# Kernel optimization log

Hardware: AMD Instinct MI355X
Metric: run time of the kernel (lower is better)

Reference implementation:

```python
import jax, jax.numpy as jnp
import numpy as np
import math

PHI = (1.0 + math.sqrt(5.0)) / 2.0
LUT_SIZE = 4096
TWO_PI = 2.0 * math.pi


def _lut_tables():
    # 4096-entry sin/cos lookup tables over [0, 2*pi)
    grid = jnp.arange(LUT_SIZE, dtype=jnp.float32) * (TWO_PI / LUT_SIZE)
    return jnp.sin(grid), jnp.cos(grid)


def _lookup_sin_cos(theta, sin_t, cos_t):
    # nearest-entry LUT lookup: index = round(theta / (2*pi) * N) mod N
    idx = jnp.mod(jnp.round(theta * (LUT_SIZE / TWO_PI)), LUT_SIZE).astype(jnp.int32)
    return sin_t[idx], cos_t[idx]


def setup_inputs() -> dict:
    key = jax.random.key(0)
    ks = jax.random.split(key, 6)
    B, D, H = 16, 2048, 2048
    return {
        "current_state_real": jax.random.normal(ks[0], (B, D), jnp.float32),
        "current_state_imag": jax.random.normal(ks[1], (B, D), jnp.float32),
        "history_real": jax.random.normal(ks[2], (B, H, D), jnp.float32),
        "history_imag": jax.random.normal(ks[3], (B, H, D), jnp.float32),
        "ema_state": jax.random.normal(ks[4], (B, 2 * D), jnp.float32),
        "w_q": jax.random.normal(ks[5], (D,), jnp.float32) * 0.02,
        "b_q": jnp.zeros((D,), jnp.float32),
        "alpha": jnp.asarray(0.1, jnp.float32),
        "t": jnp.asarray(3.0, jnp.float32),
    }


def reference(current_state_real, current_state_imag, history_real, history_imag,
              ema_state, w_q, b_q, alpha, t):
    D = current_state_real.shape[-1]
    scale = math.sqrt(2.0 * D)
    sin_t, cos_t = _lut_tables()

    wl_q = 1.0 + jnp.abs(w_q)                      # (D,)
    t_phi = t * PHI
    theta_real = current_state_real / wl_q + b_q + t_phi   # (B, D)
    theta_imag = current_state_imag / wl_q + b_q + t_phi   # (B, D)
    _, cos_q_real = _lookup_sin_cos(theta_real, sin_t, cos_t)
    _, cos_q_imag = _lookup_sin_cos(theta_imag, sin_t, cos_t)

    # keys == values == stacked history (no projection): (B, H, 2D)
    keys = jnp.concatenate([history_real, history_imag], axis=-1)
    query_for_match = jnp.concatenate([cos_q_real, cos_q_imag], axis=-1)  # (B, 2D)

    scores = jnp.einsum('bd,bhd->bh', query_for_match, keys) / scale      # (B, H)
    weights = jax.nn.softmax(scores, axis=-1)
    retrieved = jnp.einsum('bh,bhd->bd', weights, keys)                   # (B, 2D)

    a = jax.nn.sigmoid(alpha)
    new_ema = a * retrieved + (1.0 - a) * ema_state
    return new_ema
```

## Files before the change

kernel.cpp:

```cpp
#include <hip/hip_runtime.h>
#include <math.h>

#ifndef M_PI
#define M_PI 3.14159265358979323846
#endif

#define LUT_N 4096

__device__ __forceinline__ float lut_cos(float theta) {
    const float IDX_SCALE = (float)((double)LUT_N / (2.0 * M_PI));
    const float STEP = (float)((2.0 * M_PI) / (double)LUT_N);
    float x = theta * IDX_SCALE;
    int i = (int)rintf(x);
    i &= (LUT_N - 1);
    return cosf((float)i * STEP);
}

__global__ void qgen_kernel(const float* __restrict__ cur_r,
                            const float* __restrict__ cur_i,
                            const float* __restrict__ w_q,
                            const float* __restrict__ b_q,
                            const float* __restrict__ t_ptr,
                            float* __restrict__ q_out,
                            int B, int D) {
    int idx = blockIdx.x * blockDim.x + threadIdx.x;
    int twoD = 2 * D;
    if (idx >= B * twoD) return;
    int b = idx / twoD;
    int c = idx - b * twoD;
    int col = (c < D) ? c : c - D;
    const float* src = (c < D) ? cur_r : cur_i;
    float v = src[(size_t)b * D + col];
    float t_phi = t_ptr[0] * 1.61803398874989484820f;
    float wl = 1.0f + fabsf(w_q[col]);
    float theta = v / wl + b_q[col] + t_phi;
    q_out[idx] = lut_cos(theta);
}

__global__ __launch_bounds__(256) void flash_kernel(
    const float* __restrict__ hist_r,
    const float* __restrict__ hist_i,
    const float* __restrict__ q_ws,
    float* __restrict__ r_ws,
    float* __restrict__ ml_ws,
    int H, int D, int S) {
    const int t = threadIdx.x;
    const int b = blockIdx.x / S;
    const int s = blockIdx.x - b * S;
    const int rows = H / S;
    const int h0 = s * rows;
    const int Dv = D >> 2;

    const float4* qv4 = (const float4*)q_ws + (size_t)b * (D >> 1);
    float4 qv[4], rv[4];
#pragma unroll
    for (int j = 0; j < 4; ++j) {
        qv[j] = qv4[t + 256 * j];
        rv[j] = make_float4(0.f, 0.f, 0.f, 0.f);
    }
    const float4* hr4 = (const float4*)hist_r + (size_t)b * H * Dv;
    const float4* hi4 = (const float4*)hist_i + (size_t)b * H * Dv;

    float m = -INFINITY, l = 0.0f;
    const float inv_scale = 1.0f / sqrtf(2.0f * (float)D);
    __shared__ float red[4];

    for (int hh = 0; hh < rows; ++hh) {
        const size_t ro = (size_t)(h0 + hh) * Dv;
        float4 kv[4];
        kv[0] = hr4[ro + t];
        kv[1] = hr4[ro + t + 256];
        kv[2] = hi4[ro + t];
        kv[3] = hi4[ro + t + 256];
        float p = 0.f;
#pragma unroll
        for (int j = 0; j < 4; ++j)
            p += qv[j].x * kv[j].x + qv[j].y * kv[j].y +
                 qv[j].z * kv[j].z + qv[j].w * kv[j].w;
#pragma unroll
        for (int off = 32; off > 0; off >>= 1) p += __shfl_down(p, off);
        if ((t & 63) == 0) red[t >> 6] = p;
        __syncthreads();
        float sc = (red[0] + red[1] + red[2] + red[3]) * inv_scale;
        __syncthreads();
        float m_new = fmaxf(m, sc);
        float corr = expf(m - m_new);
        float w = expf(sc - m_new);
        l = fmaf(l, corr, w);
#pragma unroll
        for (int j = 0; j < 4; ++j) {
            rv[j].x = fmaf(rv[j].x, corr, w * kv[j].x);
            rv[j].y = fmaf(rv[j].y, corr, w * kv[j].y);
            rv[j].z = fmaf(rv[j].z, corr, w * kv[j].z);
            rv[j].w = fmaf(rv[j].w, corr, w * kv[j].w);
        }
        m = m_new;
    }
    float4* rout = (float4*)r_ws + (size_t)(b * S + s) * (D >> 1);
#pragma unroll
    for (int j = 0; j < 4; ++j) rout[t + 256 * j] = rv[j];
    if (t == 0) {
        ml_ws[(size_t)(b * S + s) * 2] = m;
        ml_ws[(size_t)(b * S + s) * 2 + 1] = l;
    }
}

__global__ void combine_kernel(const float* __restrict__ r_ws,
                               const float* __restrict__ ml_ws,
                               const float* __restrict__ ema,
                               const float* __restrict__ alpha_ptr,
                               float* __restrict__ out,
                               int D, int S) {
    const int twoD = 2 * D;
    const int nc = twoD / 256;
    const int b = blockIdx.x / nc;
    const int cb = blockIdx.x - b * nc;
    const int c = cb * 256 + threadIdx.x;

    const float* ml = ml_ws + (size_t)b * S * 2;
    float M = -INFINITY;
    for (int s = 0; s < S; ++s) M = fmaxf(M, ml[2 * s]);
    float L = 0.f;
    for (int s = 0; s < S; ++s) L += ml[2 * s + 1] * expf(ml[2 * s] - M);

    float acc = 0.f;
    const float* rb = r_ws + (size_t)b * S * twoD + c;
    for (int s = 0; s < S; ++s)
        acc = fmaf(expf(ml[2 * s] - M), rb[(size_t)s * twoD], acc);

    float a = 1.0f / (1.0f + expf(-alpha_ptr[0]));
    float retrieved = acc / L;
    size_t o = (size_t)b * twoD + c;
    out[o] = a * retrieved + (1.0f - a) * ema[o];
}

extern "C" void kernel_launch(void* const* d_in, const int* in_sizes, int n_in,
                              void* d_out, int out_size, void* d_ws, size_t ws_size,
                              hipStream_t stream) {
    const float* cur_r  = (const float*)d_in[0];
    const float* cur_i  = (const float*)d_in[1];
    const float* hist_r = (const float*)d_in[2];
    const float* hist_i = (const float*)d_in[3];
    const float* ema    = (const float*)d_in[4];
    const float* w_q    = (const float*)d_in[5];
    const float* b_q    = (const float*)d_in[6];
    const float* alpha  = (const float*)d_in[7];
    const float* t      = (const float*)d_in[8];

    const int D = in_sizes[5];
    const int B = in_sizes[0] / D;
    const int H = in_sizes[2] / (B * D);
    const int twoD = 2 * D;

    float* q_ws = (float*)d_ws;
    size_t q_elems = (size_t)B * twoD;

    int S = 64;
    while (S > 1) {
        size_t need = (q_elems + (size_t)B * S * twoD + (size_t)B * S * 2) * sizeof(float);
        if (need <= ws_size) break;
        S >>= 1;
    }
    float* r_ws = q_ws + q_elems;
    float* ml_ws = r_ws + (size_t)B * S * twoD;

    int qblocks = (B * twoD + 255) / 256;
    qgen_kernel<<<qblocks, 256, 0, stream>>>(cur_r, cur_i, w_q, b_q, t, q_ws, B, D);
    flash_kernel<<<B * S, 256, 0, stream>>>(hist_r, hist_i, q_ws, r_ws, ml_ws, H, D, S);
    combine_kernel<<<B * (twoD / 256), 256, 0, stream>>>(r_ws, ml_ws, ema, alpha,
                                                         (float*)d_out, D, S);
}
```

Before: 139.2 us.

## Widen flash kernel to 1024 threads and batch rows per barrier

The split-softmax attention kernel now uses 1024-thread blocks, each thread owning one float4 of the 2D row, and processes four history rows per barrier using double-buffered shared partial sums. The aim is to cut the per-row __syncthreads cost and to keep more independent loads in flight. The split count drops from 64 to 32 to keep the block count reasonable. D is now hardcoded to 2048 (the scale is fixed at 1/64 and the row stride at 512 float4s), and the loop assumes rows divisible by 4, so other shapes would break.

```diff
diff --git a/kernel.cpp b/kernel.cpp
--- a/kernel.cpp
+++ b/kernel.cpp
@@ -6,6 +6,7 @@
 #endif
 
 #define LUT_N 4096
+#define RBATCH 4
 
 __device__ __forceinline__ float lut_cos(float theta) {
     const float IDX_SCALE = (float)((double)LUT_N / (2.0 * M_PI));
@@ -37,68 +38,72 @@
     q_out[idx] = lut_cos(theta);
 }
 
-__global__ __launch_bounds__(256) void flash_kernel(
+__global__ __launch_bounds__(1024, 8) void flash_kernel(
     const float* __restrict__ hist_r,
     const float* __restrict__ hist_i,
     const float* __restrict__ q_ws,
     float* __restrict__ r_ws,
     float* __restrict__ ml_ws,
-    int H, int D, int S) {
+    int H, int S) {
     const int t = threadIdx.x;
     const int b = blockIdx.x / S;
     const int s = blockIdx.x - b * S;
     const int rows = H / S;
     const int h0 = s * rows;
-    const int Dv = D >> 2;
 
-    const float4* qv4 = (const float4*)q_ws + (size_t)b * (D >> 1);
-    float4 qv[4], rv[4];
+    const int half = t >> 9;
+    const int cc = t & 511;
+    const int wave = t >> 6, lane = t & 63;
+
+    const float4* base = (const float4*)(half ? hist_i : hist_r)
+                         + ((size_t)b * H + h0) * 512 + cc;
+    float4 qv = ((const float4*)q_ws)[(size_t)b * 1024 + t];
+    float4 rv = make_float4(0.f, 0.f, 0.f, 0.f);
+    float m = -INFINITY, l = 0.0f;
+    const float inv_scale = 1.0f / 64.0f;
+
+    __shared__ float part[2][RBATCH][16];
+
+    const int nb = rows / RBATCH;
+    for (int kb = 0; kb < nb; ++kb) {
+        const float4* rp = base + (size_t)(kb * RBATCH) * 512;
+        float4 kv[RBATCH];
 #pragma unroll
-    for (int j = 0; j < 4; ++j) {
-        qv[j] = qv4[t + 256 * j];
-        rv[j] = make_float4(0.f, 0.f, 0.f, 0.f);
+        for (int i = 0; i < RBATCH; ++i) kv[i] = rp[(size_t)i * 512];
+
+#pragma unroll
+        for (int i = 0; i < RBATCH; ++i) {
+            float p = qv.x * kv[i].x + qv.y * kv[i].y +
+                      qv.z * kv[i].z + qv.w * kv[i].w;
+#pragma unroll
+            for (int off = 32; off > 0; off >>= 1) p += __shfl_down(p, off);
+            if (lane == 0) part[kb & 1][i][wave] = p;
+        }
+        __syncthreads();
+
+        const float4* pp = (const float4*)part[kb & 1];
+#pragma unroll
+        for (int i = 0; i < RBATCH; ++i) {
+            float4 a0 = pp[4 * i + 0], a1 = pp[4 * i + 1];
+            float4 a2 = pp[4 * i + 2], a3 = pp[4 * i + 3];
+            float sc = ((a0.x + a0.y) + (a0.z + a0.w)) +
+                       ((a1.x + a1.y) + (a1.z + a1.w)) +
+                       ((a2.x + a2.y) + (a2.z + a2.w)) +
+                       ((a3.x + a3.y) + (a3.z + a3.w));
+            sc *= inv_scale;
+            float m_new = fmaxf(m, sc);
+            float corr = expf(m - m_new);
+            float w = expf(sc - m_new);
+            l = fmaf(l, corr, w);
+            rv.x = fmaf(rv.x, corr, w * kv[i].x);
+            rv.y = fmaf(rv.y, corr, w * kv[i].y);
+            rv.z = fmaf(rv.z, corr, w * kv[i].z);
+            rv.w = fmaf(rv.w, corr, w * kv[i].w);
+            m = m_new;
+        }
     }
-    const float4* hr4 = (const float4*)hist_r + (size_t)b * H * Dv;
-    const float4* hi4 = (const float4*)hist_i + (size_t)b * H * Dv;
 
-    float m = -INFINITY, l = 0.0f;
-    const float inv_scale = 1.0f / sqrtf(2.0f * (float)D);
-    __shared__ float red[4];
-
-    for (int hh = 0; hh < rows; ++hh) {
-        const size_t ro = (size_t)(h0 + hh) * Dv;
-        float4 kv[4];
-        kv[0] = hr4[ro + t];
-        kv[1] = hr4[ro + t + 256];
-        kv[2] = hi4[ro + t];
-        kv[3] = hi4[ro + t + 256];
-        float p = 0.f;
-#pragma unroll
-        for (int j = 0; j < 4; ++j)
-            p += qv[j].x * kv[j].x + qv[j].y * kv[j].y +
-                 qv[j].z * kv[j].z + qv[j].w * kv[j].w;
-#pragma unroll
-        for (int off = 32; off > 0; off >>= 1) p += __shfl_down(p, off);
-        if ((t & 63) == 0) red[t >> 6] = p;
-        __syncthreads();
-        float sc = (red[0] + red[1] + red[2] + red[3]) * inv_scale;
-        __syncthreads();
-        float m_new = fmaxf(m, sc);
-        float corr = expf(m - m_new);
-        float w = expf(sc - m_new);
-        l = fmaf(l, corr, w);
-#pragma unroll
-        for (int j = 0; j < 4; ++j) {
-            rv[j].x = fmaf(rv[j].x, corr, w * kv[j].x);
-            rv[j].y = fmaf(rv[j].y, corr, w * kv[j].y);
-            rv[j].z = fmaf(rv[j].z, corr, w * kv[j].z);
-            rv[j].w = fmaf(rv[j].w, corr, w * kv[j].w);
-        }
-        m = m_new;
-    }
-    float4* rout = (float4*)r_ws + (size_t)(b * S + s) * (D >> 1);
-#pragma unroll
-    for (int j = 0; j < 4; ++j) rout[t + 256 * j] = rv[j];
+    ((float4*)r_ws)[(size_t)(b * S + s) * 1024 + t] = rv;
     if (t == 0) {
         ml_ws[(size_t)(b * S + s) * 2] = m;
         ml_ws[(size_t)(b * S + s) * 2 + 1] = l;
@@ -155,7 +160,7 @@
     float* q_ws = (float*)d_ws;
     size_t q_elems = (size_t)B * twoD;
 
-    int S = 64;
+    int S = 32;
     while (S > 1) {
         size_t need = (q_elems + (size_t)B * S * twoD + (size_t)B * S * 2) * sizeof(float);
         if (need <= ws_size) break;
@@ -166,7 +171,7 @@
 
     int qblocks = (B * twoD + 255) / 256;
     qgen_kernel<<<qblocks, 256, 0, stream>>>(cur_r, cur_i, w_q, b_q, t, q_ws, B, D);
-    flash_kernel<<<B * S, 256, 0, stream>>>(hist_r, hist_i, q_ws, r_ws, ml_ws, H, D, S);
+    flash_kernel<<<B * S, 1024, 0, stream>>>(hist_r, hist_i, q_ws, r_ws, ml_ws, H, S);
     combine_kernel<<<B * (twoD / 256), 256, 0, stream>>>(r_ws, ml_ws, ema, alpha,
                                                          (float*)d_out, D, S);
 }
```

New measurement: 124.1 us. 1.12x faster.

## Give each wavefront its own history rows in flash attention, removing per-row block syncs

Applied to the files above, without the earlier changes.

The flash kernel now assigns disjoint row ranges to each of four wavefronts. Each wave holds the full 2D query and accumulator in registers (16 float4 each), so a score needs only a wave-level xor shuffle and no per-row __syncthreads. The online softmax skips rescaling unless the max grows by more than 8, and the wave partials are merged through shared memory at the end. D is hardcoded to 2048 (scale 1/64, stride 512), split count drops to 32, and combine uses fast __expf; the cost is heavy register pressure and less generality.

```diff
diff --git a/kernel.cpp b/kernel.cpp
--- a/kernel.cpp
+++ b/kernel.cpp
@@ -6,6 +6,7 @@
 #endif
 
 #define LUT_N 4096
+#define WPB 4
 
 __device__ __forceinline__ float lut_cos(float theta) {
     const float IDX_SCALE = (float)((double)LUT_N / (2.0 * M_PI));
@@ -37,71 +38,108 @@
     q_out[idx] = lut_cos(theta);
 }
 
-__global__ __launch_bounds__(256) void flash_kernel(
+__global__ __launch_bounds__(256, 2) void flash_kernel(
     const float* __restrict__ hist_r,
     const float* __restrict__ hist_i,
     const float* __restrict__ q_ws,
     float* __restrict__ r_ws,
     float* __restrict__ ml_ws,
-    int H, int D, int S) {
+    int H, int S) {
     const int t = threadIdx.x;
+    const int lane = t & 63;
+    const int wv = t >> 6;
     const int b = blockIdx.x / S;
     const int s = blockIdx.x - b * S;
-    const int rows = H / S;
-    const int h0 = s * rows;
-    const int Dv = D >> 2;
-
-    const float4* qv4 = (const float4*)q_ws + (size_t)b * (D >> 1);
-    float4 qv[4], rv[4];
-#pragma unroll
-    for (int j = 0; j < 4; ++j) {
-        qv[j] = qv4[t + 256 * j];
-        rv[j] = make_float4(0.f, 0.f, 0.f, 0.f);
-    }
-    const float4* hr4 = (const float4*)hist_r + (size_t)b * H * Dv;
-    const float4* hi4 = (const float4*)hist_i + (size_t)b * H * Dv;
-
-    float m = -INFINITY, l = 0.0f;
-    const float inv_scale = 1.0f / sqrtf(2.0f * (float)D);
-    __shared__ float red[4];
-
-    for (int hh = 0; hh < rows; ++hh) {
-        const size_t ro = (size_t)(h0 + hh) * Dv;
-        float4 kv[4];
-        kv[0] = hr4[ro + t];
-        kv[1] = hr4[ro + t + 256];
-        kv[2] = hi4[ro + t];
-        kv[3] = hi4[ro + t + 256];
+    const int rows_blk = H / S;
+    const int R = rows_blk / WPB;
+    const int h0 = s * rows_blk + wv * R;
+
+    const float4* hr = (const float4*)hist_r + ((size_t)b * H + h0) * 512;
+    const float4* hi = (const float4*)hist_i + ((size_t)b * H + h0) * 512;
+    const float4* q4 = (const float4*)q_ws + (size_t)b * 1024;
+
+    float4 qv[16];
+#pragma unroll
+    for (int j = 0; j < 16; ++j) qv[j] = q4[j * 64 + lane];
+
+    float4 rv[16];
+#pragma unroll
+    for (int j = 0; j < 16; ++j) rv[j] = make_float4(0.f, 0.f, 0.f, 0.f);
+    float m0 = -INFINITY, l = 0.f;
+    const float inv_scale = 1.0f / 64.0f;
+
+    for (int r = 0; r < R; ++r) {
+        float4 kv[16];
+#pragma unroll
+        for (int j = 0; j < 8; ++j) kv[j] = hr[(size_t)r * 512 + j * 64 + lane];
+#pragma unroll
+        for (int j = 0; j < 8; ++j) kv[8 + j] = hi[(size_t)r * 512 + j * 64 + lane];
+
         float p = 0.f;
 #pragma unroll
-        for (int j = 0; j < 4; ++j)
+        for (int j = 0; j < 16; ++j)
             p += qv[j].x * kv[j].x + qv[j].y * kv[j].y +
                  qv[j].z * kv[j].z + qv[j].w * kv[j].w;
 #pragma unroll
-        for (int off = 32; off > 0; off >>= 1) p += __shfl_down(p, off);
-        if ((t & 63) == 0) red[t >> 6] = p;
+        for (int off = 32; off; off >>= 1) p += __shfl_xor(p, off);
+        float sc = p * inv_scale;
+
+        float d = sc - m0;
+        float w;
+        if (d > 8.0f) {
+            float corr = __expf(-d);
+            l *= corr;
+#pragma unroll
+            for (int j = 0; j < 16; ++j) {
+                rv[j].x *= corr; rv[j].y *= corr;
+                rv[j].z *= corr; rv[j].w *= corr;
+            }
+            m0 = sc;
+            w = 1.0f;
+        } else {
+            w = __expf(d);
+        }
+        l += w;
+#pragma unroll
+        for (int j = 0; j < 16; ++j) {
+            rv[j].x = fmaf(w, kv[j].x, rv[j].x);
+            rv[j].y = fmaf(w, kv[j].y, rv[j].y);
+            rv[j].z = fmaf(w, kv[j].z, rv[j].z);
+            rv[j].w = fmaf(w, kv[j].w, rv[j].w);
+        }
+    }
+
+    __shared__ float4 sred[1024];
+    __shared__ float sm[WPB], sl[WPB];
+    if (lane == 0) { sm[wv] = m0; sl[wv] = l; }
+    __syncthreads();
+    float M = fmaxf(fmaxf(sm[0], sm[1]), fmaxf(sm[2], sm[3]));
+    float Lb = sl[0] * __expf(sm[0] - M) + sl[1] * __expf(sm[1] - M) +
+               sl[2] * __expf(sm[2] - M) + sl[3] * __expf(sm[3] - M);
+    float scale = __expf(m0 - M);
+
+    for (int w = 0; w < WPB; ++w) {
+        if (wv == w) {
+#pragma unroll
+            for (int j = 0; j < 16; ++j) {
+                int idx = j * 64 + lane;
+                float4 v = (w == 0) ? make_float4(0.f, 0.f, 0.f, 0.f) : sred[idx];
+                v.x = fmaf(scale, rv[j].x, v.x);
+                v.y = fmaf(scale, rv[j].y, v.y);
+                v.z = fmaf(scale, rv[j].z, v.z);
+                v.w = fmaf(scale, rv[j].w, v.w);
+                sred[idx] = v;
+            }
+        }
         __syncthreads();
-        float sc = (red[0] + red[1] + red[2] + red[3]) * inv_scale;
-        __syncthreads();
-        float m_new = fmaxf(m, sc);
-        float corr = expf(m - m_new);
-        float w = expf(sc - m_new);
-        l = fmaf(l, corr, w);
-#pragma unroll
-        for (int j = 0; j < 4; ++j) {
-            rv[j].x = fmaf(rv[j].x, corr, w * kv[j].x);
-            rv[j].y = fmaf(rv[j].y, corr, w * kv[j].y);
-            rv[j].z = fmaf(rv[j].z, corr, w * kv[j].z);
-            rv[j].w = fmaf(rv[j].w, corr, w * kv[j].w);
-        }
-        m = m_new;
-    }
-    float4* rout = (float4*)r_ws + (size_t)(b * S + s) * (D >> 1);
-#pragma unroll
-    for (int j = 0; j < 4; ++j) rout[t + 256 * j] = rv[j];
+    }
+
+    float4* ro = (float4*)r_ws + (size_t)blockIdx.x * 1024;
+#pragma unroll
+    for (int k = 0; k < 4; ++k) ro[t + 256 * k] = sred[t + 256 * k];
     if (t == 0) {
-        ml_ws[(size_t)(b * S + s) * 2] = m;
-        ml_ws[(size_t)(b * S + s) * 2 + 1] = l;
+        ml_ws[2 * (size_t)blockIdx.x] = M;
+        ml_ws[2 * (size_t)blockIdx.x + 1] = Lb;
     }
 }
 
@@ -121,14 +159,14 @@
     float M = -INFINITY;
     for (int s = 0; s < S; ++s) M = fmaxf(M, ml[2 * s]);
     float L = 0.f;
-    for (int s = 0; s < S; ++s) L += ml[2 * s + 1] * expf(ml[2 * s] - M);
+    for (int s = 0; s < S; ++s) L += ml[2 * s + 1] * __expf(ml[2 * s] - M);
 
     float acc = 0.f;
     const float* rb = r_ws + (size_t)b * S * twoD + c;
     for (int s = 0; s < S; ++s)
-        acc = fmaf(expf(ml[2 * s] - M), rb[(size_t)s * twoD], acc);
-
-    float a = 1.0f / (1.0f + expf(-alpha_ptr[0]));
+        acc = fmaf(__expf(ml[2 * s] - M), rb[(size_t)s * twoD], acc);
+
+    float a = 1.0f / (1.0f + __expf(-alpha_ptr[0]));
     float retrieved = acc / L;
     size_t o = (size_t)b * twoD + c;
     out[o] = a * retrieved + (1.0f - a) * ema[o];
@@ -155,7 +193,7 @@
     float* q_ws = (float*)d_ws;
     size_t q_elems = (size_t)B * twoD;
 
-    int S = 64;
+    int S = 32;
     while (S > 1) {
         size_t need = (q_elems + (size_t)B * S * twoD + (size_t)B * S * 2) * sizeof(float);
         if (need <= ws_size) break;
@@ -166,7 +204,7 @@
 
     int qblocks = (B * twoD + 255) / 256;
     qgen_kernel<<<qblocks, 256, 0, stream>>>(cur_r, cur_i, w_q, b_q, t, q_ws, B, D);
-    flash_kernel<<<B * S, 256, 0, stream>>>(hist_r, hist_i, q_ws, r_ws, ml_ws, H, D, S);
+    flash_kernel<<<B * S, 256, 0, stream>>>(hist_r, hist_i, q_ws, r_ws, ml_ws, H, S);
     combine_kernel<<<B * (twoD / 256), 256, 0, stream>>>(r_ws, ml_ws, ema, alpha,
                                                          (float*)d_out, D, S);
 }
```

New measurement: 126.3 us. 1.1x faster.
